# Kernel tuning notes

Hardware: AMD Instinct MI355X
Metric: run time of the kernel (lower is better)

## Reference

```python
import jax, jax.numpy as jnp
import numpy as np

B, H, W, C, N = 4, 64, 2650, 64, 680000
THR = 0.5  # model_cfg.FOREGROUND_THRESHOLD


def setup_inputs() -> dict:
    key = jax.random.key(0)
    k1, k2, k3, k4, k5, k6 = jax.random.split(key, 6)
    pts = jax.random.normal(k1, (N, 5), dtype=jnp.float32)
    bidx = jax.random.randint(k2, (N,), 0, B)
    points = pts.at[:, 0].set(bidx.astype(jnp.float32))  # col 0 = batch index
    ri_h = jax.random.randint(k3, (N, 1), 0, H)
    ri_w = jax.random.randint(k4, (N, 1), 0, W)
    ri_indices = jnp.concatenate([ri_h, ri_w], axis=1).astype(jnp.int32)
    seg_pred = jax.random.uniform(k5, (B, H, W), dtype=jnp.float32)
    range_features = jax.random.normal(k6, (B, C, H, W), dtype=jnp.float32)
    return {"points": points, "ri_indices": ri_indices,
            "seg_pred": seg_pred, "range_features": range_features}


def reference(points, ri_indices, seg_pred, range_features):
    # Fully-vectorized version of the per-batch loop: each point gathers its
    # range-image feature/seg score via a flat (b*H*W + r*W + c) index.
    Bn, Cc, Hh, Ww = range_features.shape
    feats_flat = jnp.transpose(range_features, (0, 2, 3, 1)).reshape(Bn * Hh * Ww, Cc)
    seg_flat = seg_pred.reshape(Bn * Hh * Ww)
    b = points[:, 0].astype(jnp.int32)
    flat_idx = b * (Hh * Ww) + ri_indices[:, 0].astype(jnp.int32) * Ww + ri_indices[:, 1].astype(jnp.int32)  # [N]
    mask = seg_flat[flat_idx] >= THR                    # foreground mask [N] bool
    point_feats = feats_flat[flat_idx]                  # [N, C] gather
    out = jnp.concatenate([points, point_feats], axis=1)  # [N, 5+C]
    # jit-compatible stand-in for boolean compaction: zero out background rows
    out = out * mask[:, None].astype(out.dtype)
    return out, mask
```

## Files before the change

### kernel.cpp

```cpp
#include <hip/hip_runtime.h>

#define B_   4
#define H_   64
#define W_   2650
#define C_   64
#define N_   680000
#define THR_ 0.5f
#define HW_  (H_ * W_)
#define W16_ 166
#define M2_  (B_ * H_ * W16_)
#define NB2_ (M2_ / 256)
#define W32_ 83
#define M32_ (B_ * H_ * W32_)


__global__ void zero_kernel(int* __restrict__ p) {
    p[blockIdx.x * 256 + threadIdx.x] = 0;
}

__global__ void hist_kernel(const float* __restrict__ pts,
                            const int* __restrict__ ri,
                            int* __restrict__ binarr) {
    int i = blockIdx.x * 256 + threadIdx.x;
    if (i >= N_) return;
    int b = (int)pts[(size_t)i * 5];
    int2 rc = ((const int2*)ri)[i];
    atomicAdd(&binarr[(b * H_ + rc.x) * W16_ + (rc.y >> 4)], 1);
}

__global__ void scan1_kernel(int* __restrict__ binarr, int* __restrict__ bsum) {
    __shared__ int lds[256];
    int t = threadIdx.x;
    int g = blockIdx.x * 256 + t;
    int v = binarr[g];
    lds[t] = v;
    __syncthreads();
    for (int off = 1; off < 256; off <<= 1) {
        int x = (t >= off) ? lds[t - off] : 0;
        __syncthreads();
        lds[t] += x;
        __syncthreads();
    }
    binarr[g] = lds[t] - v;
    if (t == 255) bsum[blockIdx.x] = lds[255];
}

__global__ void scan2_kernel(int* __restrict__ bsum) {
    __shared__ int lds[256];
    int t = threadIdx.x;
    int v = (t < NB2_) ? bsum[t] : 0;
    lds[t] = v;
    __syncthreads();
    for (int off = 1; off < 256; off <<= 1) {
        int x = (t >= off) ? lds[t - off] : 0;
        __syncthreads();
        lds[t] += x;
        __syncthreads();
    }
    if (t < NB2_) bsum[t] = lds[t] - v;
}

__global__ void scan3_kernel(int* __restrict__ binarr, const int* __restrict__ bsum) {
    int g = blockIdx.x * 256 + threadIdx.x;
    binarr[g] += bsum[blockIdx.x];
}

__global__ void scatter_kernel(const float* __restrict__ pts,
                               const int* __restrict__ ri,
                               const float* __restrict__ seg,
                               int* __restrict__ binarr,
                               int* __restrict__ perm) {
    int i = blockIdx.x * 256 + threadIdx.x;
    if (i >= N_) return;
    int b   = (int)pts[(size_t)i * 5];
    int2 rc = ((const int2*)ri)[i];
    int r = rc.x, c = rc.y;
    int bin = (b * H_ + r) * W16_ + (c >> 4);
    int m   = (seg[(size_t)b * HW_ + r * W_ + c] >= THR_) ? 1 : 0;
    int slot = atomicAdd(&binarr[bin], 1);
    perm[slot] = i | ((c & 31) << 20) | (m << 25);
}

__global__ __launch_bounds__(256) void gather_kernel(
    const float* __restrict__ pts,
    const float* __restrict__ feat,
    const int*   __restrict__ binarr,
    const int*   __restrict__ perm,
    float* __restrict__ out,
    float* __restrict__ mask_out)
{
    __shared__ float lds[4][64 * 34];
    __shared__ float alds[4][64 * 5];
    const int lane  = threadIdx.x & 63;
    const int wslot = threadIdx.x >> 6;
    const int win   = blockIdx.x * 4 + wslot;

    const int end   = binarr[2 * win + 1];
    const int start = (win == 0) ? 0 : binarr[2 * win - 1];
    if (start == end) return;

    const int b    = win / (H_ * W32_);
    const int rem  = win % (H_ * W32_);
    const int r    = rem / W32_;
    const int col0 = (rem % W32_) * 32;

    int cnt = min(end - start, 64);
    int rec_l = (lane < cnt) ? perm[start + lane] : 0;

    const size_t fbase = (size_t)(b * C_ + lane) * HW_ + (size_t)r * W_ + col0;
    float* dst = &lds[wslot][lane * 34];
    if (col0 + 32 <= W_) {
        const float2* s2 = (const float2*)(feat + fbase);
#pragma unroll
        for (int j = 0; j < 16; j++) {
            float2 v = s2[j];
            dst[2 * j] = v.x;
            dst[2 * j + 1] = v.y;
        }
    } else {
#pragma unroll
        for (int j = 0; j < 32; j++) {
            int col = col0 + j;
            if (col >= W_) col = W_ - 1;
            dst[j] = feat[(size_t)(b * C_ + lane) * HW_ + (size_t)r * W_ + col];
        }
    }

    float* arow = alds[wslot];
    int p0 = start;
    for (;;) {
        const int na = cnt * 5;
        for (int rbase = 0; rbase < na; rbase += 64) {
            int idx = rbase + lane;
            int pj  = idx / 5;
            int a   = idx - pj * 5;
            int pjc = (idx < na) ? pj : 0;
            int ptj = __shfl(rec_l, pjc) & 0xFFFFF;
            if (idx < na) arow[idx] = pts[(size_t)ptj * 5 + a];
        }
#pragma unroll 4
        for (int j = 0; j < cnt; j++) {
            const int rec = __shfl(rec_l, j);
            const int pt  = rec & 0xFFFFF;
            const float m = (float)((rec >> 25) & 1);
            const float f = dst[(rec >> 20) & 31];
            const size_t orow = (size_t)pt * 69;
            out[orow + 5 + lane] = f * m;
            if (lane < 5) out[orow + lane] = arow[j * 5 + lane] * m;
            if (lane == 0) mask_out[pt] = m;
        }
        p0 += cnt;
        if (p0 >= end) break;
        cnt = min(end - p0, 64);
        rec_l = (lane < cnt) ? perm[p0 + lane] : 0;
    }
}

__global__ __launch_bounds__(256) void gather_fallback(
    const float* __restrict__ pts, const int* __restrict__ ri,
    const float* __restrict__ seg, const float* __restrict__ feat,
    float* __restrict__ out, float* __restrict__ mask_out)
{
    const int lane = threadIdx.x & 63;
    const int pt   = blockIdx.x * 4 + (threadIdx.x >> 6);
    if (pt >= N_) return;
    int b = (int)pts[(size_t)pt * 5];
    int r = ri[pt * 2], c = ri[pt * 2 + 1];
    int rc = r * W_ + c;
    float m = (seg[b * HW_ + rc] >= THR_) ? 1.0f : 0.0f;
    float f = feat[(size_t)b * (C_ * HW_) + (size_t)lane * HW_ + rc];
    size_t orow = (size_t)pt * 69;
    out[orow + 5 + lane] = f * m;
    if (lane < 5) out[orow + lane] = pts[(size_t)pt * 5 + lane] * m;
    if (lane == 0) mask_out[pt] = m;
}


extern "C" void kernel_launch(void* const* d_in, const int* in_sizes, int n_in,
                              void* d_out, int out_size, void* d_ws, size_t ws_size,
                              hipStream_t stream) {
    const float* points = (const float*)d_in[0];
    const int*   ri     = (const int*)  d_in[1];
    const float* seg    = (const float*)d_in[2];
    const float* feat   = (const float*)d_in[3];

    float* out      = (float*)d_out;
    float* mask_out = (float*)d_out + (size_t)N_ * 69;

    int* binarr = (int*)d_ws;
    int* bsum   = binarr + M2_;
    int* perm   = bsum + 256;
    const size_t needed = ((size_t)M2_ + 256 + N_) * sizeof(int);
    const bool use_sort = (ws_size >= needed);

    const int nblkN = (N_ + 255) / 256;

    if (use_sort) {
        zero_kernel   <<<NB2_,    256, 0, stream>>>(binarr);
        hist_kernel   <<<nblkN,   256, 0, stream>>>(points, ri, binarr);
        scan1_kernel  <<<NB2_,    256, 0, stream>>>(binarr, bsum);
        scan2_kernel  <<<1,       256, 0, stream>>>(bsum);
        scan3_kernel  <<<NB2_,    256, 0, stream>>>(binarr, bsum);
        scatter_kernel<<<nblkN,   256, 0, stream>>>(points, ri, seg, binarr, perm);
        gather_kernel <<<M32_ / 4, 256, 0, stream>>>(points, feat, binarr, perm,
                                                     out, mask_out);
    } else {
        gather_fallback<<<(N_ + 3) / 4, 256, 0, stream>>>(points, ri, seg, feat,
                                                          out, mask_out);
    }
}
```

Measured before the change: 471.8 us.

## Sort only foreground points and zero-fill output up front

The histogram and scatter passes now skip background points, so only foreground points are sorted and gathered. Background rows are covered by a new grid-stride float4 zero-fill of the whole output and mask buffer. The gather windows shrink from 32 to 16 columns so each window matches one histogram bin, which removes the 2-bin window indexing and halves the feature tile loaded per wave. In exchange, every call writes the full output once more as dense zeros, and the number of gather waves doubles.

```diff
diff --git a/kernel.cpp b/kernel.cpp
--- a/kernel.cpp
+++ b/kernel.cpp
@@ -10,9 +10,15 @@
 #define W16_ 166
 #define M2_  (B_ * H_ * W16_)
 #define NB2_ (M2_ / 256)
-#define W32_ 83
-#define M32_ (B_ * H_ * W32_)
-
+
+
+__global__ void zero_out_kernel(float4* __restrict__ p) {
+    const size_t total = (size_t)N_ * 70 / 4;
+    size_t i = (size_t)blockIdx.x * 256 + threadIdx.x;
+    const size_t stride = (size_t)gridDim.x * 256;
+    const float4 z = {0.f, 0.f, 0.f, 0.f};
+    for (; i < total; i += stride) p[i] = z;
+}
 
 __global__ void zero_kernel(int* __restrict__ p) {
     p[blockIdx.x * 256 + threadIdx.x] = 0;
@@ -20,12 +26,14 @@
 
 __global__ void hist_kernel(const float* __restrict__ pts,
                             const int* __restrict__ ri,
+                            const float* __restrict__ seg,
                             int* __restrict__ binarr) {
     int i = blockIdx.x * 256 + threadIdx.x;
     if (i >= N_) return;
     int b = (int)pts[(size_t)i * 5];
     int2 rc = ((const int2*)ri)[i];
-    atomicAdd(&binarr[(b * H_ + rc.x) * W16_ + (rc.y >> 4)], 1);
+    if (seg[(size_t)b * HW_ + rc.x * W_ + rc.y] >= THR_)
+        atomicAdd(&binarr[(b * H_ + rc.x) * W16_ + (rc.y >> 4)], 1);
 }
 
 __global__ void scan1_kernel(int* __restrict__ binarr, int* __restrict__ bsum) {
@@ -75,10 +83,10 @@
     int b   = (int)pts[(size_t)i * 5];
     int2 rc = ((const int2*)ri)[i];
     int r = rc.x, c = rc.y;
-    int bin = (b * H_ + r) * W16_ + (c >> 4);
-    int m   = (seg[(size_t)b * HW_ + r * W_ + c] >= THR_) ? 1 : 0;
+    if (seg[(size_t)b * HW_ + r * W_ + c] < THR_) return;
+    int bin  = (b * H_ + r) * W16_ + (c >> 4);
     int slot = atomicAdd(&binarr[bin], 1);
-    perm[slot] = i | ((c & 31) << 20) | (m << 25);
+    perm[slot] = i | ((c & 15) << 20);
 }
 
 __global__ __launch_bounds__(256) void gather_kernel(
@@ -89,37 +97,37 @@
     float* __restrict__ out,
     float* __restrict__ mask_out)
 {
-    __shared__ float lds[4][64 * 34];
+    __shared__ float lds[4][64 * 17];
     __shared__ float alds[4][64 * 5];
     const int lane  = threadIdx.x & 63;
     const int wslot = threadIdx.x >> 6;
-    const int win   = blockIdx.x * 4 + wslot;
-
-    const int end   = binarr[2 * win + 1];
-    const int start = (win == 0) ? 0 : binarr[2 * win - 1];
+    const int bin   = blockIdx.x * 4 + wslot;
+
+    const int end   = binarr[bin];
+    const int start = (bin == 0) ? 0 : binarr[bin - 1];
     if (start == end) return;
 
-    const int b    = win / (H_ * W32_);
-    const int rem  = win % (H_ * W32_);
-    const int r    = rem / W32_;
-    const int col0 = (rem % W32_) * 32;
+    const int b    = bin / (H_ * W16_);
+    const int rem  = bin % (H_ * W16_);
+    const int r    = rem / W16_;
+    const int col0 = (rem % W16_) * 16;
 
     int cnt = min(end - start, 64);
     int rec_l = (lane < cnt) ? perm[start + lane] : 0;
 
     const size_t fbase = (size_t)(b * C_ + lane) * HW_ + (size_t)r * W_ + col0;
-    float* dst = &lds[wslot][lane * 34];
-    if (col0 + 32 <= W_) {
+    float* dst = &lds[wslot][lane * 17];
+    if (col0 + 16 <= W_) {
         const float2* s2 = (const float2*)(feat + fbase);
 #pragma unroll
-        for (int j = 0; j < 16; j++) {
+        for (int j = 0; j < 8; j++) {
             float2 v = s2[j];
             dst[2 * j] = v.x;
             dst[2 * j + 1] = v.y;
         }
     } else {
 #pragma unroll
-        for (int j = 0; j < 32; j++) {
+        for (int j = 0; j < 16; j++) {
             int col = col0 + j;
             if (col >= W_) col = W_ - 1;
             dst[j] = feat[(size_t)(b * C_ + lane) * HW_ + (size_t)r * W_ + col];
@@ -142,12 +150,11 @@
         for (int j = 0; j < cnt; j++) {
             const int rec = __shfl(rec_l, j);
             const int pt  = rec & 0xFFFFF;
-            const float m = (float)((rec >> 25) & 1);
-            const float f = dst[(rec >> 20) & 31];
+            const float f = dst[(rec >> 20) & 15];
             const size_t orow = (size_t)pt * 69;
-            out[orow + 5 + lane] = f * m;
-            if (lane < 5) out[orow + lane] = arow[j * 5 + lane] * m;
-            if (lane == 0) mask_out[pt] = m;
+            out[orow + 5 + lane] = f;
+            if (lane < 5) out[orow + lane] = arow[j * 5 + lane];
+            if (lane == 0) mask_out[pt] = 1.0f;
         }
         p0 += cnt;
         if (p0 >= end) break;
@@ -196,14 +203,15 @@
     const int nblkN = (N_ + 255) / 256;
 
     if (use_sort) {
-        zero_kernel   <<<NB2_,    256, 0, stream>>>(binarr);
-        hist_kernel   <<<nblkN,   256, 0, stream>>>(points, ri, binarr);
-        scan1_kernel  <<<NB2_,    256, 0, stream>>>(binarr, bsum);
-        scan2_kernel  <<<1,       256, 0, stream>>>(bsum);
-        scan3_kernel  <<<NB2_,    256, 0, stream>>>(binarr, bsum);
-        scatter_kernel<<<nblkN,   256, 0, stream>>>(points, ri, seg, binarr, perm);
-        gather_kernel <<<M32_ / 4, 256, 0, stream>>>(points, feat, binarr, perm,
-                                                     out, mask_out);
+        zero_out_kernel<<<2048,  256, 0, stream>>>((float4*)out);
+        zero_kernel   <<<NB2_,   256, 0, stream>>>(binarr);
+        hist_kernel   <<<nblkN,  256, 0, stream>>>(points, ri, seg, binarr);
+        scan1_kernel  <<<NB2_,   256, 0, stream>>>(binarr, bsum);
+        scan2_kernel  <<<1,      256, 0, stream>>>(bsum);
+        scan3_kernel  <<<NB2_,   256, 0, stream>>>(binarr, bsum);
+        scatter_kernel<<<nblkN,  256, 0, stream>>>(points, ri, seg, binarr, perm);
+        gather_kernel <<<M2_ / 4, 256, 0, stream>>>(points, feat, binarr, perm,
+                                                    out, mask_out);
     } else {
         gather_fallback<<<(N_ + 3) / 4, 256, 0, stream>>>(points, ri, seg, feat,
                                                           out, mask_out);
```

Result: faster. 429.5 us (-9.0%).
